# Kernel tuning notes

Measured on AMD Instinct MI355X. Metric: run time of the kernel, lower is better.

## Reference

```python
import jax, jax.numpy as jnp
import numpy as np

EPS = 1e-8  # torch nn.CosineSimilarity default eps


def setup_inputs() -> dict:
    key = jax.random.key(0)
    k1, k2 = jax.random.split(key)
    text_encodings = jax.random.normal(k1, (65536, 256), dtype=jnp.float32)
    label_encodings = jax.random.normal(k2, (1024, 256), dtype=jnp.float32)
    return {"text_encodings": text_encodings, "label_encodings": label_encodings}


def reference(text_encodings, label_encodings):
    # cosine_sim(x, y) = x.y / max(||x||*||y||, eps), computed as one matmul
    dots = jnp.einsum('nd,ld->nl', text_encodings, label_encodings)  # [N, L]
    tn = jnp.linalg.norm(text_encodings, axis=-1)    # [N]
    ln = jnp.linalg.norm(label_encodings, axis=-1)   # [L]
    denom = jnp.maximum(tn[:, None] * ln[None, :], EPS)
    return dots / denom
```

## Files before the change

### kernel.cpp

```cpp
#include <hip/hip_runtime.h>
#include <hip/hip_bf16.h>

#define NT 65536
#define NL 1024
#define DD 256

#define BM 128
#define BN 128
#define BK 64
#define TPB 16

typedef __attribute__((ext_vector_type(4))) float f32x4;
typedef __attribute__((ext_vector_type(8))) short bf16x8;

__device__ inline short f2bf(float x) {
    union { __hip_bfloat16 b; short s; } u;
    u.b = __float2bfloat16(x);
    return u.s;
}

__device__ inline void gload_lds16(const void* g, void* l) {
    __builtin_amdgcn_global_load_lds((const __attribute__((address_space(1))) void*)g,
                                     (__attribute__((address_space(3))) void*)l,
                                     16, 0, 0);
}

__global__ __launch_bounds__(256) void prep_k(const float* __restrict__ A,
                                              const float* __restrict__ Bm,
                                              short* __restrict__ Abf,
                                              short* __restrict__ Bbf,
                                              float* __restrict__ rt,
                                              float* __restrict__ rl) {
    int gw   = (blockIdx.x * 256 + threadIdx.x) >> 6;
    int lane = threadIdx.x & 63;
    if (gw >= NT + NL) return;
    const float* src = (gw < NT) ? (A + (size_t)gw * DD) : (Bm + (size_t)(gw - NT) * DD);
    short*       dst = (gw < NT) ? (Abf + (size_t)gw * DD) : (Bbf + (size_t)(gw - NT) * DD);
    f32x4 v = __builtin_nontemporal_load(reinterpret_cast<const f32x4*>(src) + lane);
    short4 o;
    o.x = f2bf(v[0]); o.y = f2bf(v[1]); o.z = f2bf(v[2]); o.w = f2bf(v[3]);
    reinterpret_cast<short4*>(dst)[lane] = o;
    float s = v[0]*v[0] + v[1]*v[1] + v[2]*v[2] + v[3]*v[3];
#pragma unroll
    for (int off = 32; off > 0; off >>= 1) s += __shfl_xor(s, off);
    if (lane == 0) {
        float r = 1.0f / fmaxf(sqrtf(s), 1e-20f);
        if (gw < NT) rt[gw] = r; else rl[gw - NT] = r;
    }
}

__global__ __launch_bounds__(512, 2) void cosim_bf_k(const short* __restrict__ Abf,
                                                     const short* __restrict__ Bbf,
                                                     const float* __restrict__ rt,
                                                     const float* __restrict__ rl,
                                                     float* __restrict__ C) {
    __shared__ short Bs[BN * DD];
    __shared__ short As[5][BM * BK];
    __shared__ float rnA[TPB * BM];
    __shared__ float rnB[BN];

    const int tid  = threadIdx.x;
    const int lane = tid & 63;
    const int w    = tid >> 6;
    const int wr   = w >> 2;
    const int wc   = w & 3;

    const int xcd   = blockIdx.x & 7;
    const int g2    = blockIdx.x >> 3;
    const int bx    = g2 & 7;
    const int sub   = g2 >> 3;
    const int strip = xcd * 4 + sub;
    const int m0b   = strip * (TPB * BM);
    const int l0    = bx * BN;

    {
        const int r2 = lane >> 5;
        const int ch = lane & 31;
#pragma unroll
        for (int i = 0; i < 8; ++i) {
            int rbase = w * 16 + i * 2;
            int row   = rbase + r2;
            int cg    = ch ^ (row & 7);
            gload_lds16(Bbf + (size_t)(l0 + row) * DD + cg * 8, &Bs[rbase * DD]);
        }
    }
#pragma unroll
    for (int i = 0; i < 4; ++i) {
        int r = tid + i * 512;
        rnA[r] = rt[m0b + r];
    }
    if (tid < BN) rnB[tid] = rl[l0 + tid];
    __syncthreads();

    const int r8  = lane >> 3;
    const int ch8 = lane & 7;
    const int cg8 = ch8 ^ r8;
    auto stageA = [&](int g, int buf) {
        const short* base = Abf + (size_t)(m0b + (g >> 2) * BM) * DD + (g & 3) * BK;
        short* dst = As[buf];
#pragma unroll
        for (int i = 0; i < 2; ++i) {
            int rbase = w * 16 + i * 8;
            gload_lds16(base + (size_t)(rbase + r8) * DD + cg8 * 8, &dst[rbase * BK]);
        }
    };

    stageA(0, 0); stageA(1, 1); stageA(2, 2); stageA(3, 3);
    int bread  = 0;
    int bstage = 4;

    const int fr = lane & 15;
    const int fq = lane >> 4;
    const int cc = lane & 15;

#pragma unroll 1
    for (int t = 0; t < TPB; ++t) {
        f32x4 acc[4][2] = {};
#pragma unroll
        for (int kt = 0; kt < 4; ++kt) {
            const int g = t * 4 + kt;
            if (t == 0) {
                asm volatile("s_waitcnt vmcnt(6)" ::: "memory");
            } else if (t == TPB - 1) {
                if      (kt == 0) asm volatile("s_waitcnt vmcnt(38)" ::: "memory");
                else if (kt == 1) asm volatile("s_waitcnt vmcnt(36)" ::: "memory");
                else if (kt == 2) asm volatile("s_waitcnt vmcnt(34)" ::: "memory");
                else              asm volatile("s_waitcnt vmcnt(32)" ::: "memory");
            } else {
                asm volatile("s_waitcnt vmcnt(38)" ::: "memory");
            }
            __builtin_amdgcn_s_barrier();

            if (t < TPB - 1) stageA(g + 4, bstage);
            bstage = (bstage == 4) ? 0 : bstage + 1;

            const short* A_ = As[bread];
            bread = (bread == 4) ? 0 : bread + 1;
#pragma unroll
            for (int ks = 0; ks < 2; ++ks) {
                bf16x8 af[4], bf2[2];
#pragma unroll
                for (int i = 0; i < 4; ++i) {
                    int row = wr * 64 + i * 16 + fr;
                    int ck  = (ks * 4 + fq) ^ (row & 7);
                    af[i] = *reinterpret_cast<const bf16x8*>(&A_[row * BK + ck * 8]);
                }
#pragma unroll
                for (int j = 0; j < 2; ++j) {
                    int row = wc * 32 + j * 16 + fr;
                    int c   = kt * 8 + ks * 4 + fq;
                    int ck  = c ^ (row & 7);
                    bf2[j] = *reinterpret_cast<const bf16x8*>(&Bs[row * DD + ck * 8]);
                }
#pragma unroll
                for (int i = 0; i < 4; ++i)
#pragma unroll
                    for (int j = 0; j < 2; ++j)
                        acc[i][j] = __builtin_amdgcn_mfma_f32_16x16x32_bf16(
                            af[i], bf2[j], acc[i][j], 0, 0, 0);
            }
        }

        const int m0 = m0b + t * BM;
#pragma unroll
        for (int i = 0; i < 4; ++i) {
#pragma unroll
            for (int rr = 0; rr < 4; ++rr) {
                int lr = wr * 64 + i * 16 + fq * 4 + rr;
                float rs = rnA[t * BM + lr];
                float* crow = C + (size_t)(m0 + lr) * NL + l0;
#pragma unroll
                for (int j = 0; j < 2; ++j) {
                    int lc = wc * 32 + j * 16 + cc;
                    __builtin_nontemporal_store(acc[i][j][rr] * rs * rnB[lc], &crow[lc]);
                }
            }
        }
    }
}

__global__ __launch_bounds__(256) void norms_k(const float* __restrict__ A,
                                               const float* __restrict__ Bm,
                                               float* __restrict__ rt,
                                               float* __restrict__ rl) {
    int gw   = (blockIdx.x * 256 + threadIdx.x) >> 6;
    int lane = threadIdx.x & 63;
    if (gw >= NT + NL) return;
    const float* src = (gw < NT) ? (A + (size_t)gw * DD) : (Bm + (size_t)(gw - NT) * DD);
    float4 v = reinterpret_cast<const float4*>(src)[lane];
    float s = v.x * v.x + v.y * v.y + v.z * v.z + v.w * v.w;
#pragma unroll
    for (int off = 32; off > 0; off >>= 1) s += __shfl_xor(s, off);
    if (lane == 0) {
        float r = 1.0f / fmaxf(sqrtf(s), 1e-20f);
        if (gw < NT) rt[gw] = r; else rl[gw - NT] = r;
    }
}

__global__ __launch_bounds__(256, 2) void cosim_fused_k(const float* __restrict__ A,
                                                        const float* __restrict__ Bm,
                                                        const float* __restrict__ rt,
                                                        const float* __restrict__ rl,
                                                        float* __restrict__ C) {
    __shared__ short As[BM * BK];
    __shared__ short Bs[BN * BK];
    const int tid  = threadIdx.x;
    const int lane = tid & 63;
    const int wid  = tid >> 6;
    const int wr   = wid >> 1;
    const int wc   = wid & 1;
    const int orig = blockIdx.x;
    const int id   = (orig & 7) * (4096 / 8) + (orig >> 3);
    const int bx   = id & 7;
    const int by   = id >> 3;
    const int m0 = by * BM;
    const int l0 = bx * BN;
    const int srow = tid >> 4;
    const int sc4  = tid & 15;
    f32x4 ra[8], rb[8];
    auto loadg = [&](int kt) {
        const float* pa = A  + (size_t)m0 * DD + kt * BK;
        const float* pb = Bm + (size_t)l0 * DD + kt * BK;
#pragma unroll
        for (int i = 0; i < 8; ++i) {
            int row = srow + i * 16;
            ra[i] = reinterpret_cast<const f32x4*>(pa + (size_t)row * DD)[sc4];
            rb[i] = reinterpret_cast<const f32x4*>(pb + (size_t)row * DD)[sc4];
        }
    };
    auto stash = [&]() {
#pragma unroll
        for (int i = 0; i < 8; ++i) {
            int row = srow + i * 16;
            short4 pa, pb;
            pa.x = f2bf(ra[i][0]); pa.y = f2bf(ra[i][1]);
            pa.z = f2bf(ra[i][2]); pa.w = f2bf(ra[i][3]);
            pb.x = f2bf(rb[i][0]); pb.y = f2bf(rb[i][1]);
            pb.z = f2bf(rb[i][2]); pb.w = f2bf(rb[i][3]);
            *reinterpret_cast<short4*>(&As[row * BK + sc4 * 4]) = pa;
            *reinterpret_cast<short4*>(&Bs[row * BK + sc4 * 4]) = pb;
        }
    };
    f32x4 acc[4][4] = {};
    loadg(0);
#pragma unroll
    for (int kt = 0; kt < DD / BK; ++kt) {
        __syncthreads();
        stash();
        __syncthreads();
        if (kt < DD / BK - 1) loadg(kt + 1);
#pragma unroll
        for (int ks = 0; ks < 2; ++ks) {
            bf16x8 af[4], bfr[4];
            const int kof = ks * 32 + (lane >> 4) * 8;
            const int ar  = wr * 64 + (lane & 15);
            const int bc  = wc * 64 + (lane & 15);
#pragma unroll
            for (int i = 0; i < 4; ++i)
                af[i] = *reinterpret_cast<const bf16x8*>(&As[(ar + i * 16) * BK + kof]);
#pragma unroll
            for (int j = 0; j < 4; ++j)
                bfr[j] = *reinterpret_cast<const bf16x8*>(&Bs[(bc + j * 16) * BK + kof]);
#pragma unroll
            for (int i = 0; i < 4; ++i)
#pragma unroll
                for (int j = 0; j < 4; ++j)
                    acc[i][j] = __builtin_amdgcn_mfma_f32_16x16x32_bf16(
                        af[i], bfr[j], acc[i][j], 0, 0, 0);
        }
    }
    const int crow0 = m0 + wr * 64;
    const int ccol0 = l0 + wc * 64;
    const int rq = lane >> 4;
    const int cc = lane & 15;
#pragma unroll
    for (int i = 0; i < 4; ++i) {
#pragma unroll
        for (int r = 0; r < 4; ++r) {
            int row = crow0 + i * 16 + rq * 4 + r;
            float rsc = rt[row];
            float* crow = C + (size_t)row * NL;
#pragma unroll
            for (int j = 0; j < 4; ++j) {
                int col = ccol0 + j * 16 + cc;
                crow[col] = acc[i][j][r] * rsc * rl[col];
            }
        }
    }
}

extern "C" void kernel_launch(void* const* d_in, const int* in_sizes, int n_in,
                              void* d_out, int out_size, void* d_ws, size_t ws_size,
                              hipStream_t stream) {
    const float* A  = (const float*)d_in[0];
    const float* Bm = (const float*)d_in[1];
    float* C = (float*)d_out;

    const size_t abf_elems = (size_t)NT * DD;
    const size_t bbf_elems = (size_t)NL * DD;
    const size_t need = (abf_elems + bbf_elems) * sizeof(short)
                      + (NT + NL) * sizeof(float);

    if (ws_size >= need) {
        short* Abf = (short*)d_ws;
        short* Bbf = Abf + abf_elems;
        float* rt  = (float*)(Bbf + bbf_elems);
        float* rl  = rt + NT;
        prep_k<<<(NT + NL) / 4, 256, 0, stream>>>(A, Bm, Abf, Bbf, rt, rl);
        cosim_bf_k<<<256, 512, 0, stream>>>(Abf, Bbf, rt, rl, C);
    } else {
        float* rt = (float*)d_ws;
        float* rl = rt + NT;
        norms_k<<<(NT + NL) / 4, 256, 0, stream>>>(A, Bm, rt, rl);
        cosim_fused_k<<<(NL / BN) * (NT / BM), 256, 0, stream>>>(A, Bm, rt, rl, C);
    }
}
```

Measured before the change: 336.9 us.

## Double-buffer accumulators to overlap output stores with next tile's MFMA

Keeps two accumulator sets and ping-pongs between tiles, so the stores of the previous tile's output are spread across the k-steps of the current tile instead of running as a block after each tile. The A-tile LDS ring drops from 5 to 4 buffers and the prefetch distance from 4 to 2 k-steps, with vmcnt waits recounted to match the interleaved stores. The prep kernel also switches from nontemporal to plain loads. This doubles accumulator register use under a 2-waves-per-SIMD launch bound, and the shorter prefetch distance may expose more load latency.

```diff
diff --git a/kernel.cpp b/kernel.cpp
--- a/kernel.cpp
+++ b/kernel.cpp
@@ -36,11 +36,11 @@
     if (gw >= NT + NL) return;
     const float* src = (gw < NT) ? (A + (size_t)gw * DD) : (Bm + (size_t)(gw - NT) * DD);
     short*       dst = (gw < NT) ? (Abf + (size_t)gw * DD) : (Bbf + (size_t)(gw - NT) * DD);
-    f32x4 v = __builtin_nontemporal_load(reinterpret_cast<const f32x4*>(src) + lane);
+    float4 v = reinterpret_cast<const float4*>(src)[lane];
     short4 o;
-    o.x = f2bf(v[0]); o.y = f2bf(v[1]); o.z = f2bf(v[2]); o.w = f2bf(v[3]);
+    o.x = f2bf(v.x); o.y = f2bf(v.y); o.z = f2bf(v.z); o.w = f2bf(v.w);
     reinterpret_cast<short4*>(dst)[lane] = o;
-    float s = v[0]*v[0] + v[1]*v[1] + v[2]*v[2] + v[3]*v[3];
+    float s = v.x * v.x + v.y * v.y + v.z * v.z + v.w * v.w;
 #pragma unroll
     for (int off = 32; off > 0; off >>= 1) s += __shfl_xor(s, off);
     if (lane == 0) {
@@ -55,7 +55,7 @@
                                                      const float* __restrict__ rl,
                                                      float* __restrict__ C) {
     __shared__ short Bs[BN * DD];
-    __shared__ short As[5][BM * BK];
+    __shared__ short As[4][BM * BK];
     __shared__ float rnA[TPB * BM];
     __shared__ float rnB[BN];
 
@@ -105,37 +105,59 @@
         }
     };
 
-    stageA(0, 0); stageA(1, 1); stageA(2, 2); stageA(3, 3);
-    int bread  = 0;
-    int bstage = 4;
+    stageA(0, 0);
+    stageA(1, 1);
 
     const int fr = lane & 15;
     const int fq = lane >> 4;
     const int cc = lane & 15;
-
-#pragma unroll 1
-    for (int t = 0; t < TPB; ++t) {
-        f32x4 acc[4][2] = {};
+    const f32x4 z4 = {0.f, 0.f, 0.f, 0.f};
+
+    f32x4 accA[4][2], accB[4][2];
+
+    auto store_q = [&](int tp, int i, f32x4 (&prev)[4][2]) {
+        const int m0 = m0b + tp * BM;
+#pragma unroll
+        for (int rr = 0; rr < 4; ++rr) {
+            int lr = wr * 64 + i * 16 + fq * 4 + rr;
+            float rs = rnA[tp * BM + lr];
+            float* crow = C + (size_t)(m0 + lr) * NL + l0;
+#pragma unroll
+            for (int j = 0; j < 2; ++j) {
+                int lc = wc * 32 + j * 16 + cc;
+                __builtin_nontemporal_store(prev[i][j][rr] * rs * rnB[lc], &crow[lc]);
+            }
+        }
+    };
+
+    auto tile = [&](int t, f32x4 (&acc)[4][2], f32x4 (&prev)[4][2], bool doStore) {
+#pragma unroll
+        for (int i = 0; i < 4; ++i)
+#pragma unroll
+            for (int j = 0; j < 2; ++j) acc[i][j] = z4;
+
 #pragma unroll
         for (int kt = 0; kt < 4; ++kt) {
             const int g = t * 4 + kt;
+            if (g + 2 < 4 * TPB) stageA(g + 2, (kt + 2) & 3);
             if (t == 0) {
-                asm volatile("s_waitcnt vmcnt(6)" ::: "memory");
-            } else if (t == TPB - 1) {
-                if      (kt == 0) asm volatile("s_waitcnt vmcnt(38)" ::: "memory");
-                else if (kt == 1) asm volatile("s_waitcnt vmcnt(36)" ::: "memory");
-                else if (kt == 2) asm volatile("s_waitcnt vmcnt(34)" ::: "memory");
-                else              asm volatile("s_waitcnt vmcnt(32)" ::: "memory");
+                asm volatile("s_waitcnt vmcnt(4)" ::: "memory");
+            } else if (t == 1) {
+                if (kt == 0)      asm volatile("s_waitcnt vmcnt(4)" ::: "memory");
+                else if (kt == 1) asm volatile("s_waitcnt vmcnt(12)" ::: "memory");
+                else              asm volatile("s_waitcnt vmcnt(20)" ::: "memory");
+            } else if (t == TPB - 1 && kt == 2) {
+                asm volatile("s_waitcnt vmcnt(18)" ::: "memory");
+            } else if (t == TPB - 1 && kt == 3) {
+                asm volatile("s_waitcnt vmcnt(16)" ::: "memory");
             } else {
-                asm volatile("s_waitcnt vmcnt(38)" ::: "memory");
+                asm volatile("s_waitcnt vmcnt(20)" ::: "memory");
             }
             __builtin_amdgcn_s_barrier();
 
-            if (t < TPB - 1) stageA(g + 4, bstage);
-            bstage = (bstage == 4) ? 0 : bstage + 1;
-
-            const short* A_ = As[bread];
-            bread = (bread == 4) ? 0 : bread + 1;
+            if (doStore) store_q(t - 1, kt, prev);
+
+            const short* A_ = As[kt];
 #pragma unroll
             for (int ks = 0; ks < 2; ++ks) {
                 bf16x8 af[4], bf2[2];
@@ -160,23 +182,15 @@
                             af[i], bf2[j], acc[i][j], 0, 0, 0);
             }
         }
-
-        const int m0 = m0b + t * BM;
-#pragma unroll
-        for (int i = 0; i < 4; ++i) {
-#pragma unroll
-            for (int rr = 0; rr < 4; ++rr) {
-                int lr = wr * 64 + i * 16 + fq * 4 + rr;
-                float rs = rnA[t * BM + lr];
-                float* crow = C + (size_t)(m0 + lr) * NL + l0;
-#pragma unroll
-                for (int j = 0; j < 2; ++j) {
-                    int lc = wc * 32 + j * 16 + cc;
-                    __builtin_nontemporal_store(acc[i][j][rr] * rs * rnB[lc], &crow[lc]);
-                }
-            }
-        }
-    }
+    };
+
+#pragma unroll 1
+    for (int tp = 0; tp < TPB; tp += 2) {
+        tile(tp,     accA, accB, tp > 0);
+        tile(tp + 1, accB, accA, true);
+    }
+#pragma unroll
+    for (int i = 0; i < 4; ++i) store_q(TPB - 1, i, accB);
 }
 
 __global__ __launch_bounds__(256) void norms_k(const float* __restrict__ A,
```

Result: faster. 318.7 us (-5.4%).
